# Kernel optimization log

Hardware: AMD Instinct MI355X
Metric: run time of the kernel (lower is better)

The kernel has to match this reference:

```python
import jax, jax.numpy as jnp
import numpy as np

N_NODES = 50000
N_EDGES = 800000
IN_SIZE = 64
LAYER = 64
BN_EPS = 1e-5


def setup_inputs() -> dict:
    key = jax.random.key(0)
    ks = jax.random.split(key, 8)
    x = jax.random.normal(ks[0], (N_NODES, IN_SIZE), dtype=jnp.float32)
    edge_index = jax.random.randint(ks[1], (2, N_EDGES), 0, N_NODES, dtype=jnp.int64)
    s0 = 1.0 / np.sqrt(2 * IN_SIZE)
    s1 = 1.0 / np.sqrt(LAYER)
    return {
        "x": x,
        "edge_index": edge_index,
        "W0": jax.random.normal(ks[2], (2 * IN_SIZE, LAYER), dtype=jnp.float32) * s0,
        "b0": jnp.zeros((LAYER,), jnp.float32),
        "g0": jnp.ones((LAYER,), jnp.float32),
        "beta0": jnp.zeros((LAYER,), jnp.float32),
        "W1": jax.random.normal(ks[3], (LAYER, LAYER), dtype=jnp.float32) * s1,
        "b1": jnp.zeros((LAYER,), jnp.float32),
        "g1": jnp.ones((LAYER,), jnp.float32),
        "beta1": jnp.zeros((LAYER,), jnp.float32),
        "W2": jax.random.normal(ks[4], (LAYER, LAYER), dtype=jnp.float32) * s1,
        "b2": jnp.zeros((LAYER,), jnp.float32),
        "g2": jnp.ones((LAYER,), jnp.float32),
        "beta2": jnp.zeros((LAYER,), jnp.float32),
    }


def _lin_bn_relu(h, W, b, g, beta):
    # Linear -> BatchNorm1d (training mode: batch stats over edge dim) -> ReLU
    h = h @ W + b
    mu = jnp.mean(h, axis=0)
    var = jnp.mean(jnp.square(h - mu), axis=0)  # biased var, as torch BN
    h = (h - mu) * jax.lax.rsqrt(var + BN_EPS) * g + beta
    return jax.nn.relu(h)


def reference(x, edge_index, W0, b0, g0, beta0, W1, b1, g1, beta1, W2, b2, g2, beta2):
    src, dst = edge_index[0], edge_index[1]
    # PyG source_to_target: x_i = x[dst] (target), x_j = x[src] (source)
    x_i = x[dst]
    x_j = x[src]
    h = jnp.concatenate([x_i, x_j], axis=-1)  # [E, 2*in]
    h = _lin_bn_relu(h, W0, b0, g0, beta0)
    h = _lin_bn_relu(h, W1, b1, g1, beta1)
    edge_activations = _lin_bn_relu(h, W2, b2, g2, beta2)  # [E, layer]
    # scatter-mean onto target nodes
    summed = jax.ops.segment_sum(edge_activations, dst, num_segments=N_NODES)
    counts = jax.ops.segment_sum(jnp.ones((edge_activations.shape[0],), edge_activations.dtype), dst, num_segments=N_NODES)
    out = summed / jnp.maximum(counts, 1.0)[:, None]
    return out, edge_activations
```

## Files before the change

kernel.cpp:

```cpp
#include <hip/hip_runtime.h>
#include <hip/hip_bf16.h>

#define E_EDGES 800000
#define NN 50000
#define BN_EPS 1e-5f

typedef __bf16 bf16x8 __attribute__((ext_vector_type(8)));
typedef __bf16 bf16x4 __attribute__((ext_vector_type(4)));
typedef float f32x4 __attribute__((ext_vector_type(4)));

__global__ void k_prep(const float* __restrict__ W0, const float* __restrict__ W1,
                       const float* __restrict__ W2, __bf16* __restrict__ W0t_top,
                       __bf16* __restrict__ W0t_bot, __bf16* __restrict__ Wt1,
                       __bf16* __restrict__ Wt2)
{
    for (int i = threadIdx.x; i < 4096; i += 256) {
        const int n = i >> 6, k = i & 63;
        W0t_top[n * 64 + k] = (__bf16)W0[k * 64 + n];
        W0t_bot[n * 64 + k] = (__bf16)W0[(64 + k) * 64 + n];
        Wt1[n * 64 + k] = (__bf16)W1[k * 64 + n];
        Wt2[n * 64 + k] = (__bf16)W2[k * 64 + n];
    }
}

__global__ __launch_bounds__(256) void k_count(
    const int* __restrict__ ei, int* __restrict__ counts)
{
    const int e = blockIdx.x * 256 + threadIdx.x;
    atomicAdd(&counts[ei[E_EDGES + e]], 1);
}

__global__ __launch_bounds__(256) void k_scan(
    const int* __restrict__ counts, int* __restrict__ offsets,
    int* __restrict__ cursor)
{
    const int CHUNK = (NN + 255) / 256;
    const int t = threadIdx.x;
    const int beg = t * CHUNK;
    const int end = (beg + CHUNK < NN) ? beg + CHUNK : NN;
    int mysum = 0;
    for (int i = beg; i < end; ++i) mysum += counts[i];

    __shared__ int sd[256];
    sd[t] = mysum;
    __syncthreads();
    int run = mysum;
    for (int off = 1; off < 256; off <<= 1) {
        int v = (t >= off) ? sd[t - off] : 0;
        __syncthreads();
        sd[t] += v;
        __syncthreads();
    }
    int prefix = sd[t] - run;
    for (int i = beg; i < end; ++i) {
        offsets[i] = prefix;
        cursor[i] = prefix;
        prefix += counts[i];
    }
}

__global__ __launch_bounds__(256) void k_gemm_node(
    const float* __restrict__ x, const __bf16* __restrict__ W0t_top,
    const __bf16* __restrict__ W0t_bot, __bf16* __restrict__ P,
    __bf16* __restrict__ Q)
{
    const int wave = threadIdx.x >> 6;
    const int grp = blockIdx.x * 4 + wave;
    if (grp >= NN / 16) return;
    const int lane = threadIdx.x & 63;
    const int quad = lane >> 4, lr = lane & 15;

    bf16x8 aT[4][2], aB[4][2];
#pragma unroll
    for (int mt = 0; mt < 4; ++mt)
#pragma unroll
        for (int s = 0; s < 2; ++s) {
            const int off = (mt * 16 + lr) * 64 + s * 32 + quad * 8;
            aT[mt][s] = *(const bf16x8*)(W0t_top + off);
            aB[mt][s] = *(const bf16x8*)(W0t_bot + off);
        }

    const int node = grp * 16 + lr;
    bf16x8 bx[2];
#pragma unroll
    for (int s = 0; s < 2; ++s) {
        const float4* ap = (const float4*)(x + (size_t)node * 64 + s * 32 + quad * 8);
        const float4 v0 = ap[0], v1 = ap[1];
        bx[s][0] = (__bf16)v0.x; bx[s][1] = (__bf16)v0.y;
        bx[s][2] = (__bf16)v0.z; bx[s][3] = (__bf16)v0.w;
        bx[s][4] = (__bf16)v1.x; bx[s][5] = (__bf16)v1.y;
        bx[s][6] = (__bf16)v1.z; bx[s][7] = (__bf16)v1.w;
    }

    f32x4 accP[4], accQ[4];
#pragma unroll
    for (int mt = 0; mt < 4; ++mt) {
        accP[mt] = (f32x4){0.f, 0.f, 0.f, 0.f};
        accQ[mt] = (f32x4){0.f, 0.f, 0.f, 0.f};
    }
#pragma unroll
    for (int s = 0; s < 2; ++s)
#pragma unroll
        for (int mt = 0; mt < 4; ++mt) {
            accP[mt] = __builtin_amdgcn_mfma_f32_16x16x32_bf16(aT[mt][s], bx[s], accP[mt], 0, 0, 0);
            accQ[mt] = __builtin_amdgcn_mfma_f32_16x16x32_bf16(aB[mt][s], bx[s], accQ[mt], 0, 0, 0);
        }

#pragma unroll
    for (int mt = 0; mt < 4; ++mt) {
        bf16x4 pv, qv;
#pragma unroll
        for (int r = 0; r < 4; ++r) { pv[r] = (__bf16)accP[mt][r]; qv[r] = (__bf16)accQ[mt][r]; }
        const size_t o = (size_t)node * 64 + mt * 16 + quad * 4;
        *(bf16x4*)(P + o) = pv;
        *(bf16x4*)(Q + o) = qv;
    }
}

__global__ __launch_bounds__(256) void k_fill_stats(
    const int* __restrict__ ei, int* __restrict__ cursor,
    const __bf16* __restrict__ P, const __bf16* __restrict__ Q,
    int4* __restrict__ rec, float* __restrict__ sums)
{
    float sa[32], sq[32];
#pragma unroll
    for (int j = 0; j < 32; ++j) { sa[j] = 0.f; sq[j] = 0.f; }

    const int lane = threadIdx.x & 63;
    const int stride = gridDim.x * 256;
    for (int s = blockIdx.x * 256 + threadIdx.x; s < 2 * E_EDGES; s += stride) {
        const int e = s >> 1, half = s & 1;
        const int src = ei[e];
        const int dst = ei[E_EDGES + e];
        int pos = 0;
        if (half == 0) pos = atomicAdd(&cursor[dst], 1);
        pos = __shfl(pos, lane & ~1);

        const bf16x8* pp = (const bf16x8*)(P + (size_t)dst * 64 + half * 32);
        const bf16x8* qp = (const bf16x8*)(Q + (size_t)src * 64 + half * 32);
        bf16x8 pf0 = pp[0], pf1 = pp[1], pf2 = pp[2], pf3 = pp[3];
        bf16x8 qf0 = qp[0], qf1 = qp[1], qf2 = qp[2], qf3 = qp[3];

        if (half == 0) rec[pos] = make_int4(e, src, dst, 0);

        float v[32];
#pragma unroll
        for (int j = 0; j < 8; ++j) {
            v[j]      = (float)pf0[j] + (float)qf0[j];
            v[8 + j]  = (float)pf1[j] + (float)qf1[j];
            v[16 + j] = (float)pf2[j] + (float)qf2[j];
            v[24 + j] = (float)pf3[j] + (float)qf3[j];
        }
#pragma unroll
        for (int j = 0; j < 32; ++j) { sa[j] += v[j]; sq[j] = fmaf(v[j], v[j], sq[j]); }
    }

#pragma unroll
    for (int off = 2; off < 64; off <<= 1)
#pragma unroll
        for (int j = 0; j < 32; ++j) {
            sa[j] += __shfl_xor(sa[j], off);
            sq[j] += __shfl_xor(sq[j], off);
        }

    __shared__ float red[4][128];
    const int wave = threadIdx.x >> 6;
    if (lane < 2) {
        const int cbase = lane * 32;
#pragma unroll
        for (int j = 0; j < 32; ++j) {
            red[wave][cbase + j] = sa[j];
            red[wave][64 + cbase + j] = sq[j];
        }
    }
    __syncthreads();
    if (threadIdx.x < 128) {
        float v2 = red[0][threadIdx.x] + red[1][threadIdx.x] + red[2][threadIdx.x] + red[3][threadIdx.x];
        atomicAdd(&sums[threadIdx.x], v2);
    }
}

__global__ __launch_bounds__(256) void k_gemm_mid1(
    const __bf16* __restrict__ P, const __bf16* __restrict__ Q,
    const int4* __restrict__ rec, __bf16* __restrict__ tout,
    const __bf16* __restrict__ Wt, const float* __restrict__ sums_in,
    const float* __restrict__ g, const float* __restrict__ beta,
    float* __restrict__ sums_out)
{
    __shared__ float clds[128];
    __shared__ float sred[4][64], qred[4][64];
    if (threadIdx.x < 64) {
        const float inv_e = 1.f / (float)E_EDGES;
        const float mu = sums_in[threadIdx.x] * inv_e;
        const float var = sums_in[64 + threadIdx.x] * inv_e - mu * mu;
        const float a = g[threadIdx.x] * rsqrtf(var + BN_EPS);
        clds[threadIdx.x] = a;
        clds[64 + threadIdx.x] = beta[threadIdx.x] - mu * a;
    }
    __syncthreads();

    const int wave = threadIdx.x >> 6;
    const int lane = threadIdx.x & 63;
    const int quad = lane >> 4, lr = lane & 15;

    float ar[2][8], cr[2][8];
#pragma unroll
    for (int s = 0; s < 2; ++s)
#pragma unroll
        for (int j = 0; j < 8; ++j) {
            const int k = s * 32 + quad * 8 + j;
            ar[s][j] = clds[k];
            cr[s][j] = clds[64 + k];
        }

    bf16x8 af[4][2];
#pragma unroll
    for (int mt = 0; mt < 4; ++mt)
#pragma unroll
        for (int s = 0; s < 2; ++s)
            af[mt][s] = *(const bf16x8*)(Wt + (mt * 16 + lr) * 64 + s * 32 + quad * 8);

    float ss[16], sq[16];
#pragma unroll
    for (int i = 0; i < 16; ++i) { ss[i] = 0.f; sq[i] = 0.f; }

    const int WAVES = 1250 * 4;
    int grp = blockIdx.x * 4 + wave;
    size_t ebase = (size_t)(grp * 16 + lr) * 64;

    int4 rc = rec[grp * 16 + lr];
    bf16x8 pcur0 = *(const bf16x8*)(P + (size_t)rc.z * 64 + quad * 8);
    bf16x8 pcur1 = *(const bf16x8*)(P + (size_t)rc.z * 64 + 32 + quad * 8);
    bf16x8 qcur0 = *(const bf16x8*)(Q + (size_t)rc.y * 64 + quad * 8);
    bf16x8 qcur1 = *(const bf16x8*)(Q + (size_t)rc.y * 64 + 32 + quad * 8);
    int4 rn = rec[(grp + WAVES) * 16 + lr];

#pragma unroll 1
    for (int it = 0; it < 10; ++it) {
        bf16x8 pn0, pn1, qn0, qn1;
        int4 rn2 = rn;
        if (it < 9) {
            pn0 = *(const bf16x8*)(P + (size_t)rn.z * 64 + quad * 8);
            pn1 = *(const bf16x8*)(P + (size_t)rn.z * 64 + 32 + quad * 8);
            qn0 = *(const bf16x8*)(Q + (size_t)rn.y * 64 + quad * 8);
            qn1 = *(const bf16x8*)(Q + (size_t)rn.y * 64 + 32 + quad * 8);
        }
        if (it < 8) rn2 = rec[(grp + 2 * WAVES) * 16 + lr];

        bf16x8 bact0, bact1;
#pragma unroll
        for (int j = 0; j < 8; ++j) {
            const float v0 = (float)pcur0[j] + (float)qcur0[j];
            const float v1 = (float)pcur1[j] + (float)qcur1[j];
            bact0[j] = (__bf16)fmaxf(fmaf(v0, ar[0][j], cr[0][j]), 0.f);
            bact1[j] = (__bf16)fmaxf(fmaf(v1, ar[1][j], cr[1][j]), 0.f);
        }

        f32x4 acc[4];
#pragma unroll
        for (int mt = 0; mt < 4; ++mt) acc[mt] = (f32x4){0.f, 0.f, 0.f, 0.f};
#pragma unroll
        for (int mt = 0; mt < 4; ++mt) {
            acc[mt] = __builtin_amdgcn_mfma_f32_16x16x32_bf16(af[mt][0], bact0, acc[mt], 0, 0, 0);
            acc[mt] = __builtin_amdgcn_mfma_f32_16x16x32_bf16(af[mt][1], bact1, acc[mt], 0, 0, 0);
        }

#pragma unroll
        for (int mt = 0; mt < 4; ++mt) {
            bf16x4 pv;
#pragma unroll
            for (int r = 0; r < 4; ++r) pv[r] = (__bf16)acc[mt][r];
            *(bf16x4*)(tout + ebase + mt * 16 + quad * 4) = pv;
#pragma unroll
            for (int r = 0; r < 4; ++r) {
                const float v = acc[mt][r];
                ss[mt * 4 + r] += v;
                sq[mt * 4 + r] = fmaf(v, v, sq[mt * 4 + r]);
            }
        }

        pcur0 = pn0; pcur1 = pn1; qcur0 = qn0; qcur1 = qn1;
        rn = rn2;
        grp += WAVES;
        ebase = (size_t)(grp * 16 + lr) * 64;
    }

#pragma unroll
    for (int i = 0; i < 16; ++i) {
        ss[i] += __shfl_xor(ss[i], 1); ss[i] += __shfl_xor(ss[i], 2);
        ss[i] += __shfl_xor(ss[i], 4); ss[i] += __shfl_xor(ss[i], 8);
        sq[i] += __shfl_xor(sq[i], 1); sq[i] += __shfl_xor(sq[i], 2);
        sq[i] += __shfl_xor(sq[i], 4); sq[i] += __shfl_xor(sq[i], 8);
    }
    if (lr == 0) {
#pragma unroll
        for (int mt = 0; mt < 4; ++mt)
#pragma unroll
            for (int r = 0; r < 4; ++r) {
                sred[wave][mt * 16 + quad * 4 + r] = ss[mt * 4 + r];
                qred[wave][mt * 16 + quad * 4 + r] = sq[mt * 4 + r];
            }
    }
    __syncthreads();
    if (threadIdx.x < 64) {
        const int c = threadIdx.x;
        atomicAdd(&sums_out[c], sred[0][c] + sred[1][c] + sred[2][c] + sred[3][c]);
        atomicAdd(&sums_out[64 + c], qred[0][c] + qred[1][c] + qred[2][c] + qred[3][c]);
    }
}

__global__ __launch_bounds__(256) void k_gemm_mid(
    const __bf16* __restrict__ tin, __bf16* __restrict__ tout,
    const __bf16* __restrict__ Wt, const float* __restrict__ sums_in,
    const float* __restrict__ g, const float* __restrict__ beta,
    float* __restrict__ sums_out)
{
    __shared__ float clds[128];
    __shared__ float sred[4][64], qred[4][64];
    if (threadIdx.x < 64) {
        const float inv_e = 1.f / (float)E_EDGES;
        const float mu = sums_in[threadIdx.x] * inv_e;
        const float var = sums_in[64 + threadIdx.x] * inv_e - mu * mu;
        const float a = g[threadIdx.x] * rsqrtf(var + BN_EPS);
        clds[threadIdx.x] = a;
        clds[64 + threadIdx.x] = beta[threadIdx.x] - mu * a;
    }
    __syncthreads();

    const int wave = threadIdx.x >> 6;
    const int lane = threadIdx.x & 63;
    const int quad = lane >> 4, lr = lane & 15;

    float ar[2][8], cr[2][8];
#pragma unroll
    for (int s = 0; s < 2; ++s)
#pragma unroll
        for (int j = 0; j < 8; ++j) {
            const int k = s * 32 + quad * 8 + j;
            ar[s][j] = clds[k];
            cr[s][j] = clds[64 + k];
        }

    bf16x8 af[4][2];
#pragma unroll
    for (int mt = 0; mt < 4; ++mt)
#pragma unroll
        for (int s = 0; s < 2; ++s)
            af[mt][s] = *(const bf16x8*)(Wt + (mt * 16 + lr) * 64 + s * 32 + quad * 8);

    float ss[16], sq[16];
#pragma unroll
    for (int i = 0; i < 16; ++i) { ss[i] = 0.f; sq[i] = 0.f; }

    const int WAVES = 1250 * 4;
    int grp = blockIdx.x * 4 + wave;
    size_t ebase = (size_t)(grp * 16 + lr) * 64;

    bf16x8 bcur0 = *(const bf16x8*)(tin + ebase + quad * 8);
    bf16x8 bcur1 = *(const bf16x8*)(tin + ebase + 32 + quad * 8);

#pragma unroll 1
    for (int it = 0; it < 10; ++it) {
        const int gn = grp + WAVES;
        const size_t enext = (size_t)(gn * 16 + lr) * 64;
        bf16x8 bn0, bn1;
        if (it < 9) {
            bn0 = *(const bf16x8*)(tin + enext + quad * 8);
            bn1 = *(const bf16x8*)(tin + enext + 32 + quad * 8);
        }

        bf16x8 bact0, bact1;
#pragma unroll
        for (int j = 0; j < 8; ++j) {
            bact0[j] = (__bf16)fmaxf(fmaf((float)bcur0[j], ar[0][j], cr[0][j]), 0.f);
            bact1[j] = (__bf16)fmaxf(fmaf((float)bcur1[j], ar[1][j], cr[1][j]), 0.f);
        }

        f32x4 acc[4];
#pragma unroll
        for (int mt = 0; mt < 4; ++mt) acc[mt] = (f32x4){0.f, 0.f, 0.f, 0.f};
#pragma unroll
        for (int mt = 0; mt < 4; ++mt) {
            acc[mt] = __builtin_amdgcn_mfma_f32_16x16x32_bf16(af[mt][0], bact0, acc[mt], 0, 0, 0);
            acc[mt] = __builtin_amdgcn_mfma_f32_16x16x32_bf16(af[mt][1], bact1, acc[mt], 0, 0, 0);
        }

#pragma unroll
        for (int mt = 0; mt < 4; ++mt) {
            bf16x4 pv;
#pragma unroll
            for (int r = 0; r < 4; ++r) pv[r] = (__bf16)acc[mt][r];
            *(bf16x4*)(tout + ebase + mt * 16 + quad * 4) = pv;
#pragma unroll
            for (int r = 0; r < 4; ++r) {
                const float v = acc[mt][r];
                ss[mt * 4 + r] += v;
                sq[mt * 4 + r] = fmaf(v, v, sq[mt * 4 + r]);
            }
        }

        bcur0 = bn0; bcur1 = bn1;
        grp = gn; ebase = enext;
    }

#pragma unroll
    for (int i = 0; i < 16; ++i) {
        ss[i] += __shfl_xor(ss[i], 1); ss[i] += __shfl_xor(ss[i], 2);
        ss[i] += __shfl_xor(ss[i], 4); ss[i] += __shfl_xor(ss[i], 8);
        sq[i] += __shfl_xor(sq[i], 1); sq[i] += __shfl_xor(sq[i], 2);
        sq[i] += __shfl_xor(sq[i], 4); sq[i] += __shfl_xor(sq[i], 8);
    }
    if (lr == 0) {
#pragma unroll
        for (int mt = 0; mt < 4; ++mt)
#pragma unroll
            for (int r = 0; r < 4; ++r) {
                sred[wave][mt * 16 + quad * 4 + r] = ss[mt * 4 + r];
                qred[wave][mt * 16 + quad * 4 + r] = sq[mt * 4 + r];
            }
    }
    __syncthreads();
    if (threadIdx.x < 64) {
        const int c = threadIdx.x;
        atomicAdd(&sums_out[c], sred[0][c] + sred[1][c] + sred[2][c] + sred[3][c]);
        atomicAdd(&sums_out[64 + c], qred[0][c] + qred[1][c] + qred[2][c] + qred[3][c]);
    }
}

__global__ __launch_bounds__(256) void k_gather_apply(
    const __bf16* __restrict__ tb, const int* __restrict__ offsets,
    const int* __restrict__ counts, const int4* __restrict__ rec,
    const float* __restrict__ sums_in, const float* __restrict__ g,
    const float* __restrict__ beta, float* __restrict__ tea,
    float* __restrict__ out)
{
    __shared__ float clds[128];
    if (threadIdx.x < 64) {
        const float inv_e = 1.f / (float)E_EDGES;
        const float mu = sums_in[threadIdx.x] * inv_e;
        const float var = sums_in[64 + threadIdx.x] * inv_e - mu * mu;
        const float a = g[threadIdx.x] * rsqrtf(var + BN_EPS);
        clds[threadIdx.x] = a;
        clds[64 + threadIdx.x] = beta[threadIdx.x] - mu * a;
    }
    __syncthreads();

    const int node = blockIdx.x * 4 + (threadIdx.x >> 6);
    const int lane = threadIdx.x & 63;
    const int es = lane >> 3;
    const int cc = lane & 7;

    float a[8], c[8];
#pragma unroll
    for (int j = 0; j < 8; ++j) { a[j] = clds[cc * 8 + j]; c[j] = clds[64 + cc * 8 + j]; }

    const int beg = offsets[node];
    const int cnt = counts[node];

    float acc8[8];
#pragma unroll
    for (int j = 0; j < 8; ++j) acc8[j] = 0.f;

    for (int i = 0; i < cnt; i += 8) {
        const int sub = i + es;
        if (sub < cnt) {
            const int p = beg + sub;
            const bf16x8 v = *(const bf16x8*)(tb + (size_t)p * 64 + cc * 8);
            const int e = rec[p].x;
            float vv[8];
#pragma unroll
            for (int j = 0; j < 8; ++j)
                vv[j] = fmaxf(fmaf((float)v[j], a[j], c[j]), 0.f);
            float* rp = tea + (size_t)e * 64 + cc * 8;
            *(float4*)rp = make_float4(vv[0], vv[1], vv[2], vv[3]);
            *(float4*)(rp + 4) = make_float4(vv[4], vv[5], vv[6], vv[7]);
#pragma unroll
            for (int j = 0; j < 8; ++j) acc8[j] += vv[j];
        }
    }

#pragma unroll
    for (int j = 0; j < 8; ++j) {
        acc8[j] += __shfl_xor(acc8[j], 8);
        acc8[j] += __shfl_xor(acc8[j], 16);
        acc8[j] += __shfl_xor(acc8[j], 32);
    }
    if (lane < 8) {
        const float inv = 1.f / fmaxf((float)cnt, 1.f);
        float* op = out + (size_t)node * 64 + lane * 8;
        *(float4*)op = make_float4(acc8[0] * inv, acc8[1] * inv, acc8[2] * inv, acc8[3] * inv);
        *(float4*)(op + 4) = make_float4(acc8[4] * inv, acc8[5] * inv, acc8[6] * inv, acc8[7] * inv);
    }
}

extern "C" void kernel_launch(void* const* d_in, const int* in_sizes, int n_in,
                              void* d_out, int out_size, void* d_ws, size_t ws_size,
                              hipStream_t stream)
{
    (void)in_sizes; (void)n_in; (void)out_size; (void)ws_size;

    const float* x     = (const float*)d_in[0];
    const int*   ei    = (const int*)d_in[1];
    const float* W0    = (const float*)d_in[2];
    const float* g0    = (const float*)d_in[4];
    const float* beta0 = (const float*)d_in[5];
    const float* W1    = (const float*)d_in[6];
    const float* g1    = (const float*)d_in[8];
    const float* beta1 = (const float*)d_in[9];
    const float* W2    = (const float*)d_in[10];
    const float* g2    = (const float*)d_in[12];
    const float* beta2 = (const float*)d_in[13];

    float* out = (float*)d_out;
    float* tea = out + (size_t)NN * 64;

    char* ws = (char*)d_ws;
    int*    counts  = (int*)(ws + 0);
    int*    offsets = (int*)(ws + 200704);
    int*    cursor  = (int*)(ws + 401408);
    float*  sums0   = (float*)(ws + 602112);
    float*  sums1   = (float*)(ws + 602624);
    float*  sums2   = (float*)(ws + 603136);
    __bf16* W0t_top = (__bf16*)(ws + 603648);
    __bf16* W0t_bot = (__bf16*)(ws + 611840);
    __bf16* Wt1     = (__bf16*)(ws + 620032);
    __bf16* Wt2     = (__bf16*)(ws + 628224);
    __bf16* P       = (__bf16*)(ws + 636928);
    __bf16* Q       = (__bf16*)(ws + 7036928);
    int4*   rec     = (int4*)(ws + 13436928);
    __bf16* tb      = (__bf16*)(ws + 26236928);

    hipMemsetAsync(counts, 0, NN * sizeof(int), stream);
    hipMemsetAsync(sums0, 0, 3 * 512, stream);

    const int GB = E_EDGES / 256;

    k_prep<<<1, 256, 0, stream>>>(W0, W1, W2, W0t_top, W0t_bot, Wt1, Wt2);
    k_count<<<GB, 256, 0, stream>>>(ei, counts);
    k_scan<<<1, 256, 0, stream>>>(counts, offsets, cursor);
    k_gemm_node<<<782, 256, 0, stream>>>(x, W0t_top, W0t_bot, P, Q);

    k_fill_stats<<<1563, 256, 0, stream>>>(ei, cursor, P, Q, rec, sums0);

    k_gemm_mid1<<<1250, 256, 0, stream>>>(P, Q, rec, tb, Wt1, sums0, g0, beta0, sums1);
    k_gemm_mid<<<1250, 256, 0, stream>>>(tb, tb, Wt2, sums1, g1, beta1, sums2);

    k_gather_apply<<<NN / 4, 256, 0, stream>>>(tb, offsets, counts, rec,
                                               sums2, g2, beta2, tea, out);
}
```

Before: 646.1 us.

## Fuse setup kernels, parallelize prefix scan, and split edge records

Two memsets and the weight-prep kernel become one zeroing/prep kernel. The edge-count and node-GEMM kernels are merged into a single launch. The single-block serial scan is replaced by a two-kernel multi-block scan. The 16-byte edge record is split into an int2 (src,dst) array plus a separate edge-index array, so the gather loops read less data. The aim is fewer launches and a shorter serial scan, in exchange for one extra scan launch and redundant block-sum scans in every block.

```diff
diff --git a/kernel.cpp b/kernel.cpp
--- a/kernel.cpp
+++ b/kernel.cpp
@@ -9,63 +9,41 @@
 typedef __bf16 bf16x4 __attribute__((ext_vector_type(4)));
 typedef float f32x4 __attribute__((ext_vector_type(4)));
 
-__global__ void k_prep(const float* __restrict__ W0, const float* __restrict__ W1,
-                       const float* __restrict__ W2, __bf16* __restrict__ W0t_top,
-                       __bf16* __restrict__ W0t_bot, __bf16* __restrict__ Wt1,
-                       __bf16* __restrict__ Wt2)
-{
-    for (int i = threadIdx.x; i < 4096; i += 256) {
-        const int n = i >> 6, k = i & 63;
-        W0t_top[n * 64 + k] = (__bf16)W0[k * 64 + n];
-        W0t_bot[n * 64 + k] = (__bf16)W0[(64 + k) * 64 + n];
-        Wt1[n * 64 + k] = (__bf16)W1[k * 64 + n];
-        Wt2[n * 64 + k] = (__bf16)W2[k * 64 + n];
-    }
-}
-
-__global__ __launch_bounds__(256) void k_count(
-    const int* __restrict__ ei, int* __restrict__ counts)
-{
-    const int e = blockIdx.x * 256 + threadIdx.x;
-    atomicAdd(&counts[ei[E_EDGES + e]], 1);
-}
-
-__global__ __launch_bounds__(256) void k_scan(
-    const int* __restrict__ counts, int* __restrict__ offsets,
-    int* __restrict__ cursor)
-{
-    const int CHUNK = (NN + 255) / 256;
-    const int t = threadIdx.x;
-    const int beg = t * CHUNK;
-    const int end = (beg + CHUNK < NN) ? beg + CHUNK : NN;
-    int mysum = 0;
-    for (int i = beg; i < end; ++i) mysum += counts[i];
-
-    __shared__ int sd[256];
-    sd[t] = mysum;
-    __syncthreads();
-    int run = mysum;
-    for (int off = 1; off < 256; off <<= 1) {
-        int v = (t >= off) ? sd[t - off] : 0;
-        __syncthreads();
-        sd[t] += v;
-        __syncthreads();
-    }
-    int prefix = sd[t] - run;
-    for (int i = beg; i < end; ++i) {
-        offsets[i] = prefix;
-        cursor[i] = prefix;
-        prefix += counts[i];
-    }
-}
-
-__global__ __launch_bounds__(256) void k_gemm_node(
+__global__ __launch_bounds__(256) void k_prep_zero(
+    const float* __restrict__ W0, const float* __restrict__ W1,
+    const float* __restrict__ W2, __bf16* __restrict__ W0t_top,
+    __bf16* __restrict__ W0t_bot, __bf16* __restrict__ Wt1,
+    __bf16* __restrict__ Wt2, int* __restrict__ counts,
+    float* __restrict__ sums_all)
+{
+    const int i = blockIdx.x * 256 + threadIdx.x;
+    if (i < NN) counts[i] = 0;
+    if (blockIdx.x == 0) {
+        for (int j = threadIdx.x; j < 384; j += 256) sums_all[j] = 0.f;
+        for (int j = threadIdx.x; j < 4096; j += 256) {
+            const int n = j >> 6, k = j & 63;
+            W0t_top[n * 64 + k] = (__bf16)W0[k * 64 + n];
+            W0t_bot[n * 64 + k] = (__bf16)W0[(64 + k) * 64 + n];
+            Wt1[n * 64 + k] = (__bf16)W1[k * 64 + n];
+            Wt2[n * 64 + k] = (__bf16)W2[k * 64 + n];
+        }
+    }
+}
+
+__global__ __launch_bounds__(256) void k_count_node(
+    const int* __restrict__ ei, int* __restrict__ counts,
     const float* __restrict__ x, const __bf16* __restrict__ W0t_top,
     const __bf16* __restrict__ W0t_bot, __bf16* __restrict__ P,
     __bf16* __restrict__ Q)
 {
+    if (blockIdx.x < 3125) {
+        const int e = blockIdx.x * 256 + threadIdx.x;
+        atomicAdd(&counts[ei[E_EDGES + e]], 1);
+        return;
+    }
+
     const int wave = threadIdx.x >> 6;
-    const int grp = blockIdx.x * 4 + wave;
+    const int grp = (blockIdx.x - 3125) * 4 + wave;
     if (grp >= NN / 16) return;
     const int lane = threadIdx.x & 63;
     const int quad = lane >> 4, lr = lane & 15;
@@ -117,10 +95,59 @@
     }
 }
 
+__global__ __launch_bounds__(256) void k_scanA(
+    const int* __restrict__ counts, int* __restrict__ bsum)
+{
+    const int i = blockIdx.x * 256 + threadIdx.x;
+    int c = (i < NN) ? counts[i] : 0;
+#pragma unroll
+    for (int off = 1; off < 64; off <<= 1) c += __shfl_xor(c, off);
+    __shared__ int sw[4];
+    if ((threadIdx.x & 63) == 0) sw[threadIdx.x >> 6] = c;
+    __syncthreads();
+    if (threadIdx.x == 0) bsum[blockIdx.x] = sw[0] + sw[1] + sw[2] + sw[3];
+}
+
+__global__ __launch_bounds__(256) void k_scanB(
+    const int* __restrict__ counts, const int* __restrict__ bsum,
+    int* __restrict__ offsets, int* __restrict__ cursor)
+{
+    const int t = threadIdx.x;
+    const int b = blockIdx.x;
+
+    __shared__ int sb[256];
+    sb[t] = (t < 196) ? bsum[t] : 0;
+    __syncthreads();
+    for (int off = 1; off < 256; off <<= 1) {
+        int v = (t >= off) ? sb[t - off] : 0;
+        __syncthreads();
+        sb[t] += v;
+        __syncthreads();
+    }
+    const int blockpre = (b == 0) ? 0 : sb[b - 1];
+
+    const int i = b * 256 + t;
+    const int c = (i < NN) ? counts[i] : 0;
+    __shared__ int sd[256];
+    sd[t] = c;
+    __syncthreads();
+    for (int off = 1; off < 256; off <<= 1) {
+        int v = (t >= off) ? sd[t - off] : 0;
+        __syncthreads();
+        sd[t] += v;
+        __syncthreads();
+    }
+    if (i < NN) {
+        const int o = blockpre + sd[t] - c;
+        offsets[i] = o;
+        cursor[i] = o;
+    }
+}
+
 __global__ __launch_bounds__(256) void k_fill_stats(
     const int* __restrict__ ei, int* __restrict__ cursor,
     const __bf16* __restrict__ P, const __bf16* __restrict__ Q,
-    int4* __restrict__ rec, float* __restrict__ sums)
+    int2* __restrict__ rec2, int* __restrict__ eidx, float* __restrict__ sums)
 {
     float sa[32], sq[32];
 #pragma unroll
@@ -141,7 +168,10 @@
         bf16x8 pf0 = pp[0], pf1 = pp[1], pf2 = pp[2], pf3 = pp[3];
         bf16x8 qf0 = qp[0], qf1 = qp[1], qf2 = qp[2], qf3 = qp[3];
 
-        if (half == 0) rec[pos] = make_int4(e, src, dst, 0);
+        if (half == 0) {
+            rec2[pos] = make_int2(src, dst);
+            eidx[pos] = e;
+        }
 
         float v[32];
 #pragma unroll
@@ -182,7 +212,7 @@
 
 __global__ __launch_bounds__(256) void k_gemm_mid1(
     const __bf16* __restrict__ P, const __bf16* __restrict__ Q,
-    const int4* __restrict__ rec, __bf16* __restrict__ tout,
+    const int2* __restrict__ rec2, __bf16* __restrict__ tout,
     const __bf16* __restrict__ Wt, const float* __restrict__ sums_in,
     const float* __restrict__ g, const float* __restrict__ beta,
     float* __restrict__ sums_out)
@@ -228,24 +258,24 @@
     int grp = blockIdx.x * 4 + wave;
     size_t ebase = (size_t)(grp * 16 + lr) * 64;
 
-    int4 rc = rec[grp * 16 + lr];
-    bf16x8 pcur0 = *(const bf16x8*)(P + (size_t)rc.z * 64 + quad * 8);
-    bf16x8 pcur1 = *(const bf16x8*)(P + (size_t)rc.z * 64 + 32 + quad * 8);
-    bf16x8 qcur0 = *(const bf16x8*)(Q + (size_t)rc.y * 64 + quad * 8);
-    bf16x8 qcur1 = *(const bf16x8*)(Q + (size_t)rc.y * 64 + 32 + quad * 8);
-    int4 rn = rec[(grp + WAVES) * 16 + lr];
+    int2 rc = rec2[grp * 16 + lr];
+    bf16x8 pcur0 = *(const bf16x8*)(P + (size_t)rc.y * 64 + quad * 8);
+    bf16x8 pcur1 = *(const bf16x8*)(P + (size_t)rc.y * 64 + 32 + quad * 8);
+    bf16x8 qcur0 = *(const bf16x8*)(Q + (size_t)rc.x * 64 + quad * 8);
+    bf16x8 qcur1 = *(const bf16x8*)(Q + (size_t)rc.x * 64 + 32 + quad * 8);
+    int2 rn = rec2[(grp + WAVES) * 16 + lr];
 
 #pragma unroll 1
     for (int it = 0; it < 10; ++it) {
         bf16x8 pn0, pn1, qn0, qn1;
-        int4 rn2 = rn;
+        int2 rn2 = rn;
         if (it < 9) {
-            pn0 = *(const bf16x8*)(P + (size_t)rn.z * 64 + quad * 8);
-            pn1 = *(const bf16x8*)(P + (size_t)rn.z * 64 + 32 + quad * 8);
-            qn0 = *(const bf16x8*)(Q + (size_t)rn.y * 64 + quad * 8);
-            qn1 = *(const bf16x8*)(Q + (size_t)rn.y * 64 + 32 + quad * 8);
-        }
-        if (it < 8) rn2 = rec[(grp + 2 * WAVES) * 16 + lr];
+            pn0 = *(const bf16x8*)(P + (size_t)rn.y * 64 + quad * 8);
+            pn1 = *(const bf16x8*)(P + (size_t)rn.y * 64 + 32 + quad * 8);
+            qn0 = *(const bf16x8*)(Q + (size_t)rn.x * 64 + quad * 8);
+            qn1 = *(const bf16x8*)(Q + (size_t)rn.x * 64 + 32 + quad * 8);
+        }
+        if (it < 8) rn2 = rec2[(grp + 2 * WAVES) * 16 + lr];
 
         bf16x8 bact0, bact1;
 #pragma unroll
@@ -429,7 +459,7 @@
 
 __global__ __launch_bounds__(256) void k_gather_apply(
     const __bf16* __restrict__ tb, const int* __restrict__ offsets,
-    const int* __restrict__ counts, const int4* __restrict__ rec,
+    const int* __restrict__ counts, const int* __restrict__ eidx,
     const float* __restrict__ sums_in, const float* __restrict__ g,
     const float* __restrict__ beta, float* __restrict__ tea,
     float* __restrict__ out)
@@ -466,7 +496,7 @@
         if (sub < cnt) {
             const int p = beg + sub;
             const bf16x8 v = *(const bf16x8*)(tb + (size_t)p * 64 + cc * 8);
-            const int e = rec[p].x;
+            const int e = eidx[p];
             float vv[8];
 #pragma unroll
             for (int j = 0; j < 8; ++j)
@@ -521,30 +551,25 @@
     float*  sums0   = (float*)(ws + 602112);
     float*  sums1   = (float*)(ws + 602624);
     float*  sums2   = (float*)(ws + 603136);
-    __bf16* W0t_top = (__bf16*)(ws + 603648);
-    __bf16* W0t_bot = (__bf16*)(ws + 611840);
-    __bf16* Wt1     = (__bf16*)(ws + 620032);
-    __bf16* Wt2     = (__bf16*)(ws + 628224);
-    __bf16* P       = (__bf16*)(ws + 636928);
-    __bf16* Q       = (__bf16*)(ws + 7036928);
-    int4*   rec     = (int4*)(ws + 13436928);
-    __bf16* tb      = (__bf16*)(ws + 26236928);
-
-    hipMemsetAsync(counts, 0, NN * sizeof(int), stream);
-    hipMemsetAsync(sums0, 0, 3 * 512, stream);
-
-    const int GB = E_EDGES / 256;
-
-    k_prep<<<1, 256, 0, stream>>>(W0, W1, W2, W0t_top, W0t_bot, Wt1, Wt2);
-    k_count<<<GB, 256, 0, stream>>>(ei, counts);
-    k_scan<<<1, 256, 0, stream>>>(counts, offsets, cursor);
-    k_gemm_node<<<782, 256, 0, stream>>>(x, W0t_top, W0t_bot, P, Q);
-
-    k_fill_stats<<<1563, 256, 0, stream>>>(ei, cursor, P, Q, rec, sums0);
-
-    k_gemm_mid1<<<1250, 256, 0, stream>>>(P, Q, rec, tb, Wt1, sums0, g0, beta0, sums1);
+    int*    bsum    = (int*)(ws + 603648);
+    __bf16* W0t_top = (__bf16*)(ws + 604672);
+    __bf16* W0t_bot = (__bf16*)(ws + 612864);
+    __bf16* Wt1     = (__bf16*)(ws + 621056);
+    __bf16* Wt2     = (__bf16*)(ws + 629248);
+    __bf16* P       = (__bf16*)(ws + 637440);
+    __bf16* Q       = (__bf16*)(ws + 7037440);
+    int2*   rec2    = (int2*)(ws + 13437440);
+    int*    eidx    = (int*)(ws + 19837440);
+    __bf16* tb      = (__bf16*)(ws + 23037440);
+
+    k_prep_zero<<<196, 256, 0, stream>>>(W0, W1, W2, W0t_top, W0t_bot, Wt1, Wt2,
+                                         counts, sums0);
+    k_count_node<<<3907, 256, 0, stream>>>(ei, counts, x, W0t_top, W0t_bot, P, Q);
+    k_scanA<<<196, 256, 0, stream>>>(counts, bsum);
+    k_scanB<<<196, 256, 0, stream>>>(counts, bsum, offsets, cursor);
+    k_fill_stats<<<1563, 256, 0, stream>>>(ei, cursor, P, Q, rec2, eidx, sums0);
+    k_gemm_mid1<<<1250, 256, 0, stream>>>(P, Q, rec2, tb, Wt1, sums0, g0, beta0, sums1);
     k_gemm_mid<<<1250, 256, 0, stream>>>(tb, tb, Wt2, sums1, g1, beta1, sums2);
-
-    k_gather_apply<<<NN / 4, 256, 0, stream>>>(tb, offsets, counts, rec,
+    k_gather_apply<<<NN / 4, 256, 0, stream>>>(tb, offsets, counts, eidx,
                                                sums2, g2, beta2, tea, out);
 }
```

After: 535.6 us, median of 2. -17.1%, faster.
